# Optimization experiments

Measured on AMD Instinct MI355X. Metric: run time of the kernel, lower is better.

The kernel has to match this reference:

```python
import jax, jax.numpy as jnp
import numpy as np

B, S, E, H = 2, 2048, 1024, 16
D = E // H  # head_dim = 64

def setup_inputs() -> dict:
    key = jax.random.key(0)
    ks = jax.random.split(key, 11)
    s = 1.0 / np.sqrt(E)
    inp = {
        'query': jax.random.normal(ks[0], (B, S, E), jnp.float32),
        'key':   jax.random.normal(ks[1], (B, S, E), jnp.float32),
        'value': jax.random.normal(ks[2], (B, S, E), jnp.float32),
        'Wq': jax.random.uniform(ks[3], (E, E), jnp.float32, -s, s),
        'bq': jax.random.uniform(ks[4], (E,), jnp.float32, -s, s),
        'Wk': jax.random.uniform(ks[5], (E, E), jnp.float32, -s, s),
        'bk': jax.random.uniform(ks[6], (E,), jnp.float32, -s, s),
        'Wv': jax.random.uniform(ks[7], (E, E), jnp.float32, -s, s),
        'bv': jax.random.uniform(ks[8], (E,), jnp.float32, -s, s),
        'Wo': jax.random.uniform(ks[9], (E, E), jnp.float32, -s, s),
        'bo': jax.random.uniform(ks[10], (E,), jnp.float32, -s, s),
    }
    return inp

def reference(query, key, value, Wq, bq, Wk, bk, Wv, bv, Wo, bo):
    # project and split heads: [B,S,E] -> [B,H,S,D]
    def proj(x, W, b):
        y = jnp.einsum('bse,fe->bsf', x, W) + b  # torch Linear: x @ W.T + b
        return y.reshape(B, S, H, D).transpose(0, 2, 1, 3)
    q = proj(query, Wq, bq)
    k = proj(key, Wk, bk)
    v = proj(value, Wv, bv)
    scores = jnp.einsum('bhqd,bhkd->bhqk', q, k) / jnp.sqrt(jnp.float32(D))
    attn = jax.nn.softmax(scores, axis=-1)
    out = jnp.einsum('bhqk,bhkd->bhqd', attn, v)  # [B,H,S,D]
    out = out.transpose(0, 2, 1, 3).reshape(B, S, E)
    return jnp.einsum('bse,fe->bsf', out, Wo) + bo
```

## Files before the change

kernel.cpp:

```cpp
#include <hip/hip_runtime.h>

#define B_ 2
#define S_ 2048
#define E_ 1024
#define H_ 16
#define D_ 64
#define M_ (B_*S_)
#define K_ E_

typedef __attribute__((ext_vector_type(8))) short  short8;
typedef __attribute__((ext_vector_type(4))) float  f32x4;
typedef __attribute__((ext_vector_type(8))) unsigned short u16x8;
typedef __attribute__((ext_vector_type(4))) unsigned short u16x4;
typedef __attribute__((ext_vector_type(4))) unsigned int   u32x4;

#define QSCALE 0.18033688011112042f

#if __has_builtin(__builtin_amdgcn_exp2f)
#define EXP2F(x) __builtin_amdgcn_exp2f(x)
#else
#define EXP2F(x) exp2f(x)
#endif

__device__ __forceinline__ unsigned short f2bf(float f) {
    unsigned u = __float_as_uint(f);
    u += 0x7fffu + ((u >> 16) & 1u);
    return (unsigned short)(u >> 16);
}

__device__ __forceinline__ void gl_lds16(const ushort* g, ushort* l) {
    __builtin_amdgcn_global_load_lds((const __attribute__((address_space(1))) void*)g,
                                     (__attribute__((address_space(3))) void*)l,
                                     16, 0, 0);
}

__global__ __launch_bounds__(256)
void cvt_all(const float* __restrict__ q, const float* __restrict__ k,
             const float* __restrict__ v, const float* __restrict__ wq,
             const float* __restrict__ wk, const float* __restrict__ wv,
             const float* __restrict__ wo, ushort* __restrict__ dst)
{
    const int bid = blockIdx.x;
    const float* src;
    size_t dof;
    int local;
    if (bid < 6144) {
        const int t = bid >> 11;
        src = (t == 0) ? q : (t == 1) ? k : v;
        dof = (size_t)t * 4194304u;
        local = bid & 2047;
    } else {
        const int r = bid - 6144;
        const int t = r >> 9;
        src = (t == 0) ? wq : (t == 1) ? wk : (t == 2) ? wv : wo;
        dof = 12582912u + (size_t)t * 1048576u;
        local = r & 511;
    }
    const size_t idx = (size_t)local * 2048 + threadIdx.x * 8;
    const float4 a = *(const float4*)(src + idx);
    const float4 b = *(const float4*)(src + idx + 4);
    u16x8 o;
    o[0] = f2bf(a.x); o[1] = f2bf(a.y); o[2] = f2bf(a.z); o[3] = f2bf(a.w);
    o[4] = f2bf(b.x); o[5] = f2bf(b.y); o[6] = f2bf(b.z); o[7] = f2bf(b.w);
    *(u16x8*)(dst + dof + idx) = o;
}

template<int SWAP>
__device__ __forceinline__ void gemm_core(const ushort* __restrict__ X,
                                          const ushort* __restrict__ W,
                                          int m0, int n0,
                                          f32x4 acc[4][4],
                                          ushort* Ast, ushort* Bst)
{
    const int tid  = threadIdx.x;
    const int lane = tid & 63;
    const int w    = tid >> 6;
    const int wm   = w & 1, wn = w >> 1;
    const int r0   = tid >> 2;
    const int c8   = (tid & 3) * 8;

    const f32x4 zero = {0.f, 0.f, 0.f, 0.f};
    #pragma unroll
    for (int mt = 0; mt < 4; ++mt)
        #pragma unroll
        for (int nt = 0; nt < 4; ++nt) acc[mt][nt] = zero;

    const int kb = (lane >> 4) * 8;

    for (int k0 = 0; k0 < K_; k0 += 32) {
        __syncthreads();
        const ushort* ga = X + (size_t)(m0 + r0) * K_ + k0 + c8;
        gl_lds16(ga, Ast + tid * 8);
        gl_lds16(ga + (size_t)64 * K_, Ast + 2048 + tid * 8);
        const ushort* gb = W + (size_t)(n0 + r0) * K_ + k0 + c8;
        gl_lds16(gb, Bst + tid * 8);
        gl_lds16(gb + (size_t)64 * K_, Bst + 2048 + tid * 8);
        __syncthreads();

        short8 af[4], bf[4];
        #pragma unroll
        for (int mt = 0; mt < 4; ++mt)
            af[mt] = *(const short8*)(Ast + (wm * 64 + mt * 16 + (lane & 15)) * 32 + kb);
        #pragma unroll
        for (int nt = 0; nt < 4; ++nt)
            bf[nt] = *(const short8*)(Bst + (wn * 64 + nt * 16 + (lane & 15)) * 32 + kb);
        #pragma unroll
        for (int mt = 0; mt < 4; ++mt)
            #pragma unroll
            for (int nt = 0; nt < 4; ++nt) {
                if (SWAP)
                    acc[mt][nt] = __builtin_amdgcn_mfma_f32_16x16x32_bf16(bf[nt], af[mt], acc[mt][nt], 0, 0, 0);
                else
                    acc[mt][nt] = __builtin_amdgcn_mfma_f32_16x16x32_bf16(af[mt], bf[nt], acc[mt][nt], 0, 0, 0);
            }
    }
}

__global__ __launch_bounds__(256)
void gemm_qkv(const ushort* __restrict__ Xq, const ushort* __restrict__ Xk,
              const ushort* __restrict__ Xv, const ushort* __restrict__ Wq,
              const ushort* __restrict__ Wk, const ushort* __restrict__ Wv,
              const float* __restrict__ bq, const float* __restrict__ bk,
              const float* __restrict__ bv, ushort* __restrict__ Qh,
              ushort* __restrict__ Kh, ushort* __restrict__ Vt)
{
    __shared__ ushort Ast[128 * 32];
    __shared__ ushort Bst[128 * 32];
    const int z = blockIdx.z;
    const ushort* X = (z == 0) ? Xq : (z == 1) ? Xk : Xv;
    const ushort* W = (z == 0) ? Wq : (z == 1) ? Wk : Wv;
    const float* bias = (z == 0) ? bq : (z == 1) ? bk : bv;
    ushort* dst = (z == 0) ? Qh : (z == 1) ? Kh : Vt;

    const int m0 = blockIdx.y * 128, n0 = blockIdx.x * 128;
    f32x4 acc[4][4];
    const int lane = threadIdx.x & 63, w = threadIdx.x >> 6;
    const int wm = w & 1, wn = w >> 1;
    const int l15 = lane & 15, quad = lane >> 4;

    if (z < 2) {
        gemm_core<1>(X, W, m0, n0, acc, Ast, Bst);
        const float qsc = (z == 0) ? QSCALE : 1.0f;
        #pragma unroll
        for (int nt = 0; nt < 4; ++nt) {
            const int nb = n0 + wn * 64 + nt * 16 + quad * 4;
            const int h = nb >> 6, d0 = nb & 63;
            const float4 b4 = *(const float4*)(bias + nb);
            const float bb4[4] = {b4.x, b4.y, b4.z, b4.w};
            #pragma unroll
            for (int mt = 0; mt < 4; ++mt) {
                const int tok = m0 + wm * 64 + mt * 16 + l15;
                const int b = tok >> 11, s = tok & (S_ - 1);
                u16x4 pk;
                #pragma unroll
                for (int r = 0; r < 4; ++r)
                    pk[r] = f2bf((acc[mt][nt][r] + bb4[r]) * qsc);
                *(u16x4*)&dst[(((size_t)(b * H_ + h) * S_) + s) * D_ + d0] = pk;
            }
        }
    } else {
        gemm_core<0>(X, W, m0, n0, acc, Ast, Bst);
        float bias4[4];
        #pragma unroll
        for (int nt = 0; nt < 4; ++nt)
            bias4[nt] = bias[n0 + wn * 64 + nt * 16 + l15];
        #pragma unroll
        for (int mt = 0; mt < 4; ++mt) {
            const int mrow0 = m0 + wm * 64 + mt * 16 + (quad * 4);
            const int b = mrow0 >> 11;
            const int s0 = mrow0 & (S_ - 1);
            #pragma unroll
            for (int nt = 0; nt < 4; ++nt) {
                const int n = n0 + wn * 64 + nt * 16 + l15;
                const int h = n >> 6, d = n & 63;
                u16x4 pk;
                #pragma unroll
                for (int r = 0; r < 4; ++r) pk[r] = f2bf(acc[mt][nt][r] + bias4[nt]);
                *(u16x4*)&Vt[(((size_t)(b * H_ + h) * D_) + d) * S_ + s0] = pk;
            }
        }
    }
}

__global__ __launch_bounds__(256)
void gemm_out(const ushort* __restrict__ X, const ushort* __restrict__ W,
              const float* __restrict__ bias, float* __restrict__ out)
{
    __shared__ ushort Ast[128 * 32];
    __shared__ ushort Bst[64 * 32];
    const int m0 = blockIdx.y * 128, n0 = blockIdx.x * 64;
    const int tid = threadIdx.x, lane = tid & 63, w = tid >> 6;
    const int wm = w & 1, wn = w >> 1;
    const int l15 = lane & 15, quad = lane >> 4;
    const int r0 = tid >> 2, c8 = (tid & 3) * 8;
    const int kb = quad * 8;

    const f32x4 zero = {0.f, 0.f, 0.f, 0.f};
    f32x4 acc[4][2];
    #pragma unroll
    for (int mt = 0; mt < 4; ++mt)
        #pragma unroll
        for (int nt = 0; nt < 2; ++nt) acc[mt][nt] = zero;

    for (int k0 = 0; k0 < K_; k0 += 32) {
        __syncthreads();
        const ushort* ga = X + (size_t)(m0 + r0) * K_ + k0 + c8;
        gl_lds16(ga, Ast + tid * 8);
        gl_lds16(ga + (size_t)64 * K_, Ast + 2048 + tid * 8);
        const ushort* gb = W + (size_t)(n0 + r0) * K_ + k0 + c8;
        gl_lds16(gb, Bst + tid * 8);
        __syncthreads();

        short8 af[4], bf[2];
        #pragma unroll
        for (int mt = 0; mt < 4; ++mt)
            af[mt] = *(const short8*)(Ast + (wm * 64 + mt * 16 + l15) * 32 + kb);
        #pragma unroll
        for (int nt = 0; nt < 2; ++nt)
            bf[nt] = *(const short8*)(Bst + (wn * 32 + nt * 16 + l15) * 32 + kb);
        #pragma unroll
        for (int mt = 0; mt < 4; ++mt)
            #pragma unroll
            for (int nt = 0; nt < 2; ++nt)
                acc[mt][nt] = __builtin_amdgcn_mfma_f32_16x16x32_bf16(af[mt], bf[nt], acc[mt][nt], 0, 0, 0);
    }

    float bias2[2];
    #pragma unroll
    for (int nt = 0; nt < 2; ++nt)
        bias2[nt] = bias[n0 + wn * 32 + nt * 16 + l15];

    #pragma unroll
    for (int mt = 0; mt < 4; ++mt) {
        const int mrow0 = m0 + wm * 64 + mt * 16 + quad * 4;
        #pragma unroll
        for (int nt = 0; nt < 2; ++nt) {
            const int n = n0 + wn * 32 + nt * 16 + l15;
            #pragma unroll
            for (int r = 0; r < 4; ++r)
                out[(size_t)(mrow0 + r) * E_ + n] = acc[mt][nt][r] + bias2[nt];
        }
    }
}

#define NTILE (S_ / 64)
__global__ __launch_bounds__(256, 3)
void flash_mfma(const ushort* __restrict__ Qg, const ushort* __restrict__ Kg,
                const ushort* __restrict__ Vg, ushort* __restrict__ AO)
{
    __shared__ ushort sh[20480];
    ushort* Qs = sh;
    ushort* K0 = sh + 4096;
    ushort* V0 = sh + 8192;
    ushort* K1 = sh + 12288;
    ushort* V1 = sh + 16384;

    const int tid = threadIdx.x, lane = tid & 63, w = tid >> 6;
    const int l15 = lane & 15, quad = lane >> 4;
    const int q0 = blockIdx.x * 64, h = blockIdx.y, b = blockIdx.z;
    const size_t qk_off = (size_t)(b * H_ + h) * S_ * D_;
    const size_t vt_off = (size_t)(b * H_ + h) * D_ * S_;

    #pragma unroll
    for (int i = 0; i < 2; ++i) {
        const int chunk = w + i * 4;
        const int row = chunk * 8 + (lane >> 3);
        const int gcol = (lane & 7) ^ (row & 7);
        gl_lds16(Qg + qk_off + (size_t)(q0 + row) * D_ + gcol * 8,
                 Qs + chunk * 512 + lane * 8);
        gl_lds16(Kg + qk_off + (size_t)row * D_ + gcol * 8,
                 K0 + chunk * 512 + lane * 8);
        gl_lds16(Vg + vt_off + (size_t)row * S_ + gcol * 8,
                 V0 + chunk * 512 + lane * 8);
    }
    __syncthreads();

    const f32x4 zero = {0.f, 0.f, 0.f, 0.f};
    f32x4 o[4][4];
    #pragma unroll
    for (int g = 0; g < 4; ++g)
        #pragma unroll
        for (int nt = 0; nt < 4; ++nt) o[g][nt] = zero;
    float lsum[4] = {0.f, 0.f, 0.f, 0.f};

    const int krow = (w * 16 + l15) * 64;
    const int gidx = (2 * w + (quad >> 1)) ^ (l15 & 7);

    for (int jp = 0; jp < NTILE; jp += 2) {
        short8 ka[2];
        #pragma unroll
        for (int kt = 0; kt < 2; ++kt)
            ka[kt] = *(const short8*)&K0[krow + (((kt * 4 + quad) ^ (l15 & 7)) * 8)];
        uint2 vvA[4];
        #pragma unroll
        for (int nt = 0; nt < 4; ++nt)
            vvA[nt] = *(const uint2*)&V0[(nt * 16 + l15) * 64 + gidx * 8 + (quad & 1) * 4];

        {
            const int j0n = (jp + 1) * 64;
            #pragma unroll
            for (int i = 0; i < 2; ++i) {
                const int chunk = w + i * 4;
                const int row = chunk * 8 + (lane >> 3);
                const int gcol = (lane & 7) ^ (row & 7);
                gl_lds16(Kg + qk_off + (size_t)(j0n + row) * D_ + gcol * 8,
                         K1 + chunk * 512 + lane * 8);
                gl_lds16(Vg + vt_off + (size_t)row * S_ + j0n + gcol * 8,
                         V1 + chunk * 512 + lane * 8);
            }
        }

        uint2 paLo[4];
        #pragma unroll
        for (int g = 0; g < 4; ++g) {
            const short8 qg0 = *(const short8*)&Qs[(g * 16 + l15) * 64 +
                                                   ((quad ^ (l15 & 7)) * 8)];
            const short8 qg1 = *(const short8*)&Qs[(g * 16 + l15) * 64 +
                                                   (((4 + quad) ^ (l15 & 7)) * 8)];
            f32x4 t;
            t = __builtin_amdgcn_mfma_f32_16x16x32_bf16(ka[0], qg0, zero, 0, 0, 0);
            t = __builtin_amdgcn_mfma_f32_16x16x32_bf16(ka[1], qg1, t, 0, 0, 0);
            const float p0 = EXP2F(t[0]), p1 = EXP2F(t[1]);
            const float p2 = EXP2F(t[2]), p3 = EXP2F(t[3]);
            lsum[g] += (p0 + p1) + (p2 + p3);
            const unsigned a0 = __float_as_uint(p0) + 0x8000u;
            const unsigned a1 = __float_as_uint(p1) + 0x8000u;
            const unsigned a2 = __float_as_uint(p2) + 0x8000u;
            const unsigned a3 = __float_as_uint(p3) + 0x8000u;
            paLo[g].x = (a1 & 0xffff0000u) | (a0 >> 16);
            paLo[g].y = (a3 & 0xffff0000u) | (a2 >> 16);
        }
        __syncthreads();

        #pragma unroll
        for (int kt = 0; kt < 2; ++kt)
            ka[kt] = *(const short8*)&K1[krow + (((kt * 4 + quad) ^ (l15 & 7)) * 8)];
        uint2 vvB[4];
        #pragma unroll
        for (int nt = 0; nt < 4; ++nt)
            vvB[nt] = *(const uint2*)&V1[(nt * 16 + l15) * 64 + gidx * 8 + (quad & 1) * 4];

        if (jp + 2 < NTILE) {
            const int j0n = (jp + 2) * 64;
            #pragma unroll
            for (int i = 0; i < 2; ++i) {
                const int chunk = w + i * 4;
                const int row = chunk * 8 + (lane >> 3);
                const int gcol = (lane & 7) ^ (row & 7);
                gl_lds16(Kg + qk_off + (size_t)(j0n + row) * D_ + gcol * 8,
                         K0 + chunk * 512 + lane * 8);
                gl_lds16(Vg + vt_off + (size_t)row * S_ + j0n + gcol * 8,
                         V0 + chunk * 512 + lane * 8);
            }
        }

        short8 pa8[4];
        #pragma unroll
        for (int g = 0; g < 4; ++g) {
            const short8 qg0 = *(const short8*)&Qs[(g * 16 + l15) * 64 +
                                                   ((quad ^ (l15 & 7)) * 8)];
            const short8 qg1 = *(const short8*)&Qs[(g * 16 + l15) * 64 +
                                                   (((4 + quad) ^ (l15 & 7)) * 8)];
            f32x4 t;
            t = __builtin_amdgcn_mfma_f32_16x16x32_bf16(ka[0], qg0, zero, 0, 0, 0);
            t = __builtin_amdgcn_mfma_f32_16x16x32_bf16(ka[1], qg1, t, 0, 0, 0);
            const float p0 = EXP2F(t[0]), p1 = EXP2F(t[1]);
            const float p2 = EXP2F(t[2]), p3 = EXP2F(t[3]);
            lsum[g] += (p0 + p1) + (p2 + p3);
            const unsigned a0 = __float_as_uint(p0) + 0x8000u;
            const unsigned a1 = __float_as_uint(p1) + 0x8000u;
            const unsigned a2 = __float_as_uint(p2) + 0x8000u;
            const unsigned a3 = __float_as_uint(p3) + 0x8000u;
            u32x4 pk;
            pk[0] = paLo[g].x;
            pk[1] = paLo[g].y;
            pk[2] = (a1 & 0xffff0000u) | (a0 >> 16);
            pk[3] = (a3 & 0xffff0000u) | (a2 >> 16);
            pa8[g] = __builtin_bit_cast(short8, pk);
        }

        #pragma unroll
        for (int nt = 0; nt < 4; ++nt) {
            u32x4 vk;
            vk[0] = vvA[nt].x; vk[1] = vvA[nt].y;
            vk[2] = vvB[nt].x; vk[3] = vvB[nt].y;
            const short8 vb8 = __builtin_bit_cast(short8, vk);
            #pragma unroll
            for (int g = 0; g < 4; ++g)
                o[g][nt] = __builtin_amdgcn_mfma_f32_16x16x32_bf16(pa8[g], vb8, o[g][nt], 0, 0, 0);
        }

        __syncthreads();
    }

    #pragma unroll
    for (int g = 0; g < 4; ++g) {
        lsum[g] += __shfl_xor(lsum[g], 16);
        lsum[g] += __shfl_xor(lsum[g], 32);
    }
    __syncthreads();
    float* fb = (float*)sh;
    #pragma unroll
    for (int g = 0; g < 4; ++g) {
        if (w != g) {
            #pragma unroll
            for (int nt = 0; nt < 4; ++nt)
                #pragma unroll
                for (int r = 0; r < 4; ++r)
                    fb[w * 1024 + (nt * 4 + r) * 64 + lane] = o[g][nt][r];
            if (quad == 0) fb[4096 + w * 64 + l15] = lsum[g];
        }
        __syncthreads();
        if (w == g) {
            #pragma unroll
            for (int ws = 0; ws < 4; ++ws) {
                if (ws == g) continue;
                #pragma unroll
                for (int nt = 0; nt < 4; ++nt)
                    #pragma unroll
                    for (int r = 0; r < 4; ++r)
                        o[g][nt][r] += fb[ws * 1024 + (nt * 4 + r) * 64 + lane];
                lsum[g] += fb[4096 + ws * 64 + l15];
            }
        }
        __syncthreads();
    }

    #pragma unroll
    for (int g = 0; g < 4; ++g) {
        if (w == g) {
            const float inv = 1.0f / lsum[g];
            float invr[4];
            #pragma unroll
            for (int r = 0; r < 4; ++r)
                invr[r] = __shfl(inv, (lane & 0x30) | (quad * 4 + r));
            #pragma unroll
            for (int nt = 0; nt < 4; ++nt) {
                const int e = h * 64 + nt * 16 + l15;
                #pragma unroll
                for (int r = 0; r < 4; ++r) {
                    const int s = q0 + g * 16 + quad * 4 + r;
                    AO[(size_t)(b * S_ + s) * E_ + e] = f2bf(o[g][nt][r] * invr[r]);
                }
            }
        }
    }
}

extern "C" void kernel_launch(void* const* d_in, const int* in_sizes, int n_in,
                              void* d_out, int out_size, void* d_ws, size_t ws_size,
                              hipStream_t stream) {
    const float* query = (const float*)d_in[0];
    const float* key   = (const float*)d_in[1];
    const float* value = (const float*)d_in[2];
    const float* Wq = (const float*)d_in[3];
    const float* bq = (const float*)d_in[4];
    const float* Wk = (const float*)d_in[5];
    const float* bk = (const float*)d_in[6];
    const float* Wv = (const float*)d_in[7];
    const float* bv = (const float*)d_in[8];
    const float* Wo = (const float*)d_in[9];
    const float* bo = (const float*)d_in[10];
    float* out = (float*)d_out;

    ushort* ws = (ushort*)d_ws;
    ushort* Xq  = ws;
    ushort* Xk  = ws + 4194304u;
    ushort* Xv  = ws + 8388608u;
    ushort* Wqb = ws + 12582912u;
    ushort* Wkb = ws + 13631488u;
    ushort* Wvb = ws + 14680064u;
    ushort* Wob = ws + 15728640u;
    ushort* Qh  = ws + 16777216u;
    ushort* Kh  = ws + 20971520u;
    ushort* Vt  = ws + 25165824u;
    ushort* AO  = ws + 29360128u;

    cvt_all<<<8192, 256, 0, stream>>>(query, key, value, Wq, Wk, Wv, Wo, ws);
    gemm_qkv<<<dim3(8, 32, 3), 256, 0, stream>>>(Xq, Xk, Xv, Wqb, Wkb, Wvb,
                                                 bq, bk, bv, Qh, Kh, Vt);
    flash_mfma<<<dim3(32, 16, 2), 256, 0, stream>>>(Qh, Kh, Vt, AO);
    gemm_out<<<dim3(16, 32), 256, 0, stream>>>(AO, Wob, bo, out);
}
```

Before: 232.2 us.

## Fuse activation bf16 conversion into QKV GEMM and hoist Q fragments into registers

The separate conversion pass over the fp32 query/key/value activations is removed. The QKV GEMM now loads fp32 A tiles directly, converts them to bf16 in registers and stores them to LDS, which avoids writing and re-reading a bf16 copy of the activations. Each activation element is now converted about eight times, once per N tile, and the A-side loads become synchronous register loads instead of direct global-to-LDS loads. Separately, the flash kernel keeps its Q fragments in registers for the whole kernel instead of re-reading LDS every tile, and its occupancy hint drops from 3 to 2 to leave room for the extra registers.

```diff
diff --git a/kernel.cpp b/kernel.cpp
--- a/kernel.cpp
+++ b/kernel.cpp
@@ -35,27 +35,15 @@
 }
 
 __global__ __launch_bounds__(256)
-void cvt_all(const float* __restrict__ q, const float* __restrict__ k,
-             const float* __restrict__ v, const float* __restrict__ wq,
-             const float* __restrict__ wk, const float* __restrict__ wv,
-             const float* __restrict__ wo, ushort* __restrict__ dst)
+void cvt_w(const float* __restrict__ wq, const float* __restrict__ wk,
+           const float* __restrict__ wv, const float* __restrict__ wo,
+           ushort* __restrict__ dst)
 {
     const int bid = blockIdx.x;
-    const float* src;
-    size_t dof;
-    int local;
-    if (bid < 6144) {
-        const int t = bid >> 11;
-        src = (t == 0) ? q : (t == 1) ? k : v;
-        dof = (size_t)t * 4194304u;
-        local = bid & 2047;
-    } else {
-        const int r = bid - 6144;
-        const int t = r >> 9;
-        src = (t == 0) ? wq : (t == 1) ? wk : (t == 2) ? wv : wo;
-        dof = 12582912u + (size_t)t * 1048576u;
-        local = r & 511;
-    }
+    const int t = bid >> 9;
+    const int local = bid & 511;
+    const float* src = (t == 0) ? wq : (t == 1) ? wk : (t == 2) ? wv : wo;
+    const size_t dof = (size_t)t * 1048576u;
     const size_t idx = (size_t)local * 2048 + threadIdx.x * 8;
     const float4 a = *(const float4*)(src + idx);
     const float4 b = *(const float4*)(src + idx + 4);
@@ -66,11 +54,11 @@
 }
 
 template<int SWAP>
-__device__ __forceinline__ void gemm_core(const ushort* __restrict__ X,
-                                          const ushort* __restrict__ W,
-                                          int m0, int n0,
-                                          f32x4 acc[4][4],
-                                          ushort* Ast, ushort* Bst)
+__device__ __forceinline__ void gemm_core_f32a(const float* __restrict__ X,
+                                               const ushort* __restrict__ W,
+                                               int m0, int n0,
+                                               f32x4 acc[4][4],
+                                               ushort* Ast, ushort* Bst)
 {
     const int tid  = threadIdx.x;
     const int lane = tid & 63;
@@ -89,12 +77,21 @@
 
     for (int k0 = 0; k0 < K_; k0 += 32) {
         __syncthreads();
-        const ushort* ga = X + (size_t)(m0 + r0) * K_ + k0 + c8;
-        gl_lds16(ga, Ast + tid * 8);
-        gl_lds16(ga + (size_t)64 * K_, Ast + 2048 + tid * 8);
         const ushort* gb = W + (size_t)(n0 + r0) * K_ + k0 + c8;
         gl_lds16(gb, Bst + tid * 8);
         gl_lds16(gb + (size_t)64 * K_, Bst + 2048 + tid * 8);
+        const float* ga = X + (size_t)(m0 + r0) * K_ + k0 + c8;
+        const float4 a0 = *(const float4*)(ga);
+        const float4 a1 = *(const float4*)(ga + 4);
+        const float4 b0 = *(const float4*)(ga + (size_t)64 * K_);
+        const float4 b1 = *(const float4*)(ga + (size_t)64 * K_ + 4);
+        u16x8 pa, pb;
+        pa[0] = f2bf(a0.x); pa[1] = f2bf(a0.y); pa[2] = f2bf(a0.z); pa[3] = f2bf(a0.w);
+        pa[4] = f2bf(a1.x); pa[5] = f2bf(a1.y); pa[6] = f2bf(a1.z); pa[7] = f2bf(a1.w);
+        pb[0] = f2bf(b0.x); pb[1] = f2bf(b0.y); pb[2] = f2bf(b0.z); pb[3] = f2bf(b0.w);
+        pb[4] = f2bf(b1.x); pb[5] = f2bf(b1.y); pb[6] = f2bf(b1.z); pb[7] = f2bf(b1.w);
+        *(u16x8*)(Ast + tid * 8) = pa;
+        *(u16x8*)(Ast + 2048 + tid * 8) = pb;
         __syncthreads();
 
         short8 af[4], bf[4];
@@ -117,8 +114,8 @@
 }
 
 __global__ __launch_bounds__(256)
-void gemm_qkv(const ushort* __restrict__ Xq, const ushort* __restrict__ Xk,
-              const ushort* __restrict__ Xv, const ushort* __restrict__ Wq,
+void gemm_qkv(const float* __restrict__ Xq, const float* __restrict__ Xk,
+              const float* __restrict__ Xv, const ushort* __restrict__ Wq,
               const ushort* __restrict__ Wk, const ushort* __restrict__ Wv,
               const float* __restrict__ bq, const float* __restrict__ bk,
               const float* __restrict__ bv, ushort* __restrict__ Qh,
@@ -127,10 +124,9 @@
     __shared__ ushort Ast[128 * 32];
     __shared__ ushort Bst[128 * 32];
     const int z = blockIdx.z;
-    const ushort* X = (z == 0) ? Xq : (z == 1) ? Xk : Xv;
+    const float* X = (z == 0) ? Xq : (z == 1) ? Xk : Xv;
     const ushort* W = (z == 0) ? Wq : (z == 1) ? Wk : Wv;
     const float* bias = (z == 0) ? bq : (z == 1) ? bk : bv;
-    ushort* dst = (z == 0) ? Qh : (z == 1) ? Kh : Vt;
 
     const int m0 = blockIdx.y * 128, n0 = blockIdx.x * 128;
     f32x4 acc[4][4];
@@ -139,7 +135,8 @@
     const int l15 = lane & 15, quad = lane >> 4;
 
     if (z < 2) {
-        gemm_core<1>(X, W, m0, n0, acc, Ast, Bst);
+        gemm_core_f32a<1>(X, W, m0, n0, acc, Ast, Bst);
+        ushort* dst = (z == 0) ? Qh : Kh;
         const float qsc = (z == 0) ? QSCALE : 1.0f;
         #pragma unroll
         for (int nt = 0; nt < 4; ++nt) {
@@ -159,7 +156,7 @@
             }
         }
     } else {
-        gemm_core<0>(X, W, m0, n0, acc, Ast, Bst);
+        gemm_core_f32a<0>(X, W, m0, n0, acc, Ast, Bst);
         float bias4[4];
         #pragma unroll
         for (int nt = 0; nt < 4; ++nt)
@@ -244,7 +241,7 @@
 }
 
 #define NTILE (S_ / 64)
-__global__ __launch_bounds__(256, 3)
+__global__ __launch_bounds__(256, 2)
 void flash_mfma(const ushort* __restrict__ Qg, const ushort* __restrict__ Kg,
                 const ushort* __restrict__ Vg, ushort* __restrict__ AO)
 {
@@ -275,6 +272,14 @@
     }
     __syncthreads();
 
+    short8 qb[4][2];
+    #pragma unroll
+    for (int g = 0; g < 4; ++g)
+        #pragma unroll
+        for (int kt = 0; kt < 2; ++kt)
+            qb[g][kt] = *(const short8*)&Qs[(g * 16 + l15) * 64 +
+                                            (((kt * 4 + quad) ^ (l15 & 7)) * 8)];
+
     const f32x4 zero = {0.f, 0.f, 0.f, 0.f};
     f32x4 o[4][4];
     #pragma unroll
@@ -313,13 +318,9 @@
         uint2 paLo[4];
         #pragma unroll
         for (int g = 0; g < 4; ++g) {
-            const short8 qg0 = *(const short8*)&Qs[(g * 16 + l15) * 64 +
-                                                   ((quad ^ (l15 & 7)) * 8)];
-            const short8 qg1 = *(const short8*)&Qs[(g * 16 + l15) * 64 +
-                                                   (((4 + quad) ^ (l15 & 7)) * 8)];
             f32x4 t;
-            t = __builtin_amdgcn_mfma_f32_16x16x32_bf16(ka[0], qg0, zero, 0, 0, 0);
-            t = __builtin_amdgcn_mfma_f32_16x16x32_bf16(ka[1], qg1, t, 0, 0, 0);
+            t = __builtin_amdgcn_mfma_f32_16x16x32_bf16(ka[0], qb[g][0], zero, 0, 0, 0);
+            t = __builtin_amdgcn_mfma_f32_16x16x32_bf16(ka[1], qb[g][1], t, 0, 0, 0);
             const float p0 = EXP2F(t[0]), p1 = EXP2F(t[1]);
             const float p2 = EXP2F(t[2]), p3 = EXP2F(t[3]);
             lsum[g] += (p0 + p1) + (p2 + p3);
@@ -357,13 +358,9 @@
         short8 pa8[4];
         #pragma unroll
         for (int g = 0; g < 4; ++g) {
-            const short8 qg0 = *(const short8*)&Qs[(g * 16 + l15) * 64 +
-                                                   ((quad ^ (l15 & 7)) * 8)];
-            const short8 qg1 = *(const short8*)&Qs[(g * 16 + l15) * 64 +
-                                                   (((4 + quad) ^ (l15 & 7)) * 8)];
             f32x4 t;
-            t = __builtin_amdgcn_mfma_f32_16x16x32_bf16(ka[0], qg0, zero, 0, 0, 0);
-            t = __builtin_amdgcn_mfma_f32_16x16x32_bf16(ka[1], qg1, t, 0, 0, 0);
+            t = __builtin_amdgcn_mfma_f32_16x16x32_bf16(ka[0], qb[g][0], zero, 0, 0, 0);
+            t = __builtin_amdgcn_mfma_f32_16x16x32_bf16(ka[1], qb[g][1], t, 0, 0, 0);
             const float p0 = EXP2F(t[0]), p1 = EXP2F(t[1]);
             const float p2 = EXP2F(t[2]), p3 = EXP2F(t[3]);
             lsum[g] += (p0 + p1) + (p2 + p3);
@@ -464,20 +461,17 @@
     float* out = (float*)d_out;
 
     ushort* ws = (ushort*)d_ws;
-    ushort* Xq  = ws;
-    ushort* Xk  = ws + 4194304u;
-    ushort* Xv  = ws + 8388608u;
-    ushort* Wqb = ws + 12582912u;
-    ushort* Wkb = ws + 13631488u;
-    ushort* Wvb = ws + 14680064u;
-    ushort* Wob = ws + 15728640u;
-    ushort* Qh  = ws + 16777216u;
-    ushort* Kh  = ws + 20971520u;
-    ushort* Vt  = ws + 25165824u;
-    ushort* AO  = ws + 29360128u;
-
-    cvt_all<<<8192, 256, 0, stream>>>(query, key, value, Wq, Wk, Wv, Wo, ws);
-    gemm_qkv<<<dim3(8, 32, 3), 256, 0, stream>>>(Xq, Xk, Xv, Wqb, Wkb, Wvb,
+    ushort* Wqb = ws;
+    ushort* Wkb = ws + 1048576u;
+    ushort* Wvb = ws + 2097152u;
+    ushort* Wob = ws + 3145728u;
+    ushort* Qh  = ws + 4194304u;
+    ushort* Kh  = ws + 8388608u;
+    ushort* Vt  = ws + 12582912u;
+    ushort* AO  = ws + 16777216u;
+
+    cvt_w<<<2048, 256, 0, stream>>>(Wq, Wk, Wv, Wo, ws);
+    gemm_qkv<<<dim3(8, 32, 3), 256, 0, stream>>>(query, key, value, Wqb, Wkb, Wvb,
                                                  bq, bk, bv, Qh, Kh, Vt);
     flash_mfma<<<dim3(32, 16, 2), 256, 0, stream>>>(Qh, Kh, Vt, AO);
     gemm_out<<<dim3(16, 32), 256, 0, stream>>>(AO, Wob, bo, out);
```

After: 241.5 us. +4.0%, slower.
